# Kernel optimization log

Hardware: AMD Instinct MI355X
Metric: run time of the kernel (lower is better)

The kernel has to match this reference:

```python
import jax, jax.numpy as jnp
import numpy as np

N_VARS = 50000
N_EDGES = 400000
HIDDEN = 128


def setup_inputs() -> dict:
    key = jax.random.key(0)
    k1, k2, k3 = jax.random.split(key, 3)
    x = jax.random.normal(k1, (N_VARS, HIDDEN), dtype=jnp.float32)
    # torch Linear(2H, H, bias=False): weight shape [H, 2H]
    W = jax.random.normal(k2, (HIDDEN, 2 * HIDDEN), dtype=jnp.float32) * (1.0 / np.sqrt(2 * HIDDEN))
    edge_idx = jax.random.randint(k3, (2, N_EDGES), 0, N_VARS, dtype=jnp.int32)
    return {"x": x, "W": W, "edge_idx": edge_idx}


def reference(x, W, edge_idx):
    # Symmetrize edges: append reversed edges -> [2, 2E]
    src = jnp.concatenate([edge_idx[0], edge_idx[1]])  # [2E]
    dst = jnp.concatenate([edge_idx[1], edge_idx[0]])  # [2E]
    # Gather endpoint features and concat -> [2E, 2H]
    m = jnp.concatenate([x[src], x[dst]], axis=1)
    # Small dense linear (no bias): [2E, 2H] @ [2H, H] -> [2E, H]
    m = m @ W.T
    # scatter_sum over destination index, dim_size = num_vars
    r = jax.ops.segment_sum(m, dst, num_segments=x.shape[0])
    return r
```

## Files before the change

### kernel.cpp

```cpp
#include <hip/hip_runtime.h>

#define N_VARS   50000
#define N_EDGES  400000
#define HID      128
#define MTILES   (N_VARS / 16)
#define GEMM_BLOCKS ((MTILES + 1) / 2)
#define NBKT_A   196
#define CCAP     4608
#define NBKT_G   1563
#define CAP      64
#define CAPP     66
#define ABLOCKS  391

#define Y1_B0   0
#define Y1_SZ   (N_VARS * HID)
#define Y2_B0   (Y1_B0 + Y1_SZ)
#define Y2_SZ   (N_VARS * HID * 2)
#define WB_B0   (Y2_B0 + Y2_SZ)
#define WB_SZ   (64 * 64 * 8 * 2)
#define INT_B0  (WB_B0 + WB_SZ)

#define I_GCOUNT 0
#define I_COARSE (I_GCOUNT + NBKT_A)

typedef __attribute__((ext_vector_type(8))) short bf16x8;
typedef __attribute__((ext_vector_type(4))) float f32x4;
typedef __attribute__((ext_vector_type(2))) float f32x2;

__device__ __forceinline__ unsigned short f2bf(float f) {
    unsigned u = __builtin_bit_cast(unsigned, f);
    unsigned r = u + 0x7fffu + ((u >> 16) & 1u);
    return (unsigned short)(r >> 16);
}

__device__ __forceinline__ bf16x8 cvt8(float4 a0, float4 a1) {
    bf16x8 r;
    r[0] = (short)f2bf(a0.x); r[1] = (short)f2bf(a0.y);
    r[2] = (short)f2bf(a0.z); r[3] = (short)f2bf(a0.w);
    r[4] = (short)f2bf(a1.x); r[5] = (short)f2bf(a1.y);
    r[6] = (short)f2bf(a1.z); r[7] = (short)f2bf(a1.w);
    return r;
}

__global__ __launch_bounds__(256) void prep_kernel(const float* __restrict__ W,
                                                   short* __restrict__ wb,
                                                   int* __restrict__ gcount) {
    int gid = blockIdx.x * 256 + threadIdx.x;
    if (gid < NBKT_A) gcount[gid] = 0;
    if (gid < 4096) {
        int f = gid >> 6, lane = gid & 63;
        int nt = f >> 2, kc = f & 3;
        int ml = lane & 15, quad = lane >> 4;
        int n = nt * 16 + ml;
        const float* wp = (n < HID) ? (W + (size_t)n * 256)
                                    : (W + (size_t)(n - HID) * 256 + HID);
        wp += kc * 32 + quad * 8;
        const float4* w4 = (const float4*)wp;
        *(bf16x8*)(wb + (size_t)f * 512 + lane * 8) = cvt8(w4[0], w4[1]);
    }
}

__global__ __launch_bounds__(256) void gemm_binA_kernel(
    const float* __restrict__ x, const short* __restrict__ wb,
    const int* __restrict__ e,
    unsigned char* __restrict__ y1f8, unsigned short* __restrict__ y2b,
    int* __restrict__ gcount, int* __restrict__ coarse) {
    __shared__ int cnt[NBKT_A];
    __shared__ int base[NBKT_A];
    const int t = threadIdx.x;

    if (blockIdx.x < GEMM_BLOCKS) {
        const int lane = t & 63;
        const int wv   = t >> 6;
        const int ml   = lane & 15;
        const int quad = lane >> 4;

        bf16x8 bfrag[4][4];
#pragma unroll
        for (int i = 0; i < 4; ++i)
#pragma unroll
            for (int kc = 0; kc < 4; ++kc)
                bfrag[i][kc] = *(const bf16x8*)(wb + (size_t)((wv * 4 + i) * 4 + kc) * 512 + lane * 8);

#pragma unroll
        for (int mi = 0; mi < 2; ++mi) {
            const int mt = blockIdx.x * 2 + mi;
            if (mt >= MTILES) break;
            const int v = mt * 16 + ml;

            bf16x8 afrag[4];
#pragma unroll
            for (int kc = 0; kc < 4; ++kc) {
                const float4* ap = (const float4*)(x + (size_t)v * HID + kc * 32 + quad * 8);
                afrag[kc] = cvt8(ap[0], ap[1]);
            }

            f32x4 acc[4];
#pragma unroll
            for (int i = 0; i < 4; ++i) acc[i] = f32x4{0.f, 0.f, 0.f, 0.f};
#pragma unroll
            for (int kc = 0; kc < 4; ++kc)
#pragma unroll
                for (int i = 0; i < 4; ++i)
                    acc[i] = __builtin_amdgcn_mfma_f32_16x16x32_bf16(bfrag[i][kc], afrag[kc], acc[i], 0, 0, 0);

            if (wv < 2) {
#pragma unroll
                for (int i = 0; i < 4; ++i) {
                    int w = __builtin_amdgcn_cvt_pk_fp8_f32(acc[i][0], acc[i][1], 0, false);
                    w     = __builtin_amdgcn_cvt_pk_fp8_f32(acc[i][2], acc[i][3], w, true);
                    *(int*)(y1f8 + (size_t)v * HID + wv * 64 + i * 16 + quad * 4) = w;
                }
            } else {
#pragma unroll
                for (int i = 0; i < 4; ++i) {
                    uint2 p;
                    p.x = (unsigned)f2bf(acc[i][0]) | ((unsigned)f2bf(acc[i][1]) << 16);
                    p.y = (unsigned)f2bf(acc[i][2]) | ((unsigned)f2bf(acc[i][3]) << 16);
                    *(uint2*)(y2b + (size_t)v * HID + (wv - 2) * 64 + i * 16 + quad * 4) = p;
                }
            }
        }
    } else {
        const int bA = blockIdx.x - GEMM_BLOCKS;
        if (t < NBKT_A) cnt[t] = 0;
        __syncthreads();

        int e0[4], e1[4], nb = 0;
        const int b0 = (bA * 256 + t) * 4;
        if (bA < ABLOCKS - 1) {
            int4 A = *(const int4*)(e + b0);
            int4 B = *(const int4*)(e + N_EDGES + b0);
            e0[0] = A.x; e0[1] = A.y; e0[2] = A.z; e0[3] = A.w;
            e1[0] = B.x; e1[1] = B.y; e1[2] = B.z; e1[3] = B.w;
            nb = 4;
        } else {
            for (int j = 0; j < 4; ++j)
                if (b0 + j < N_EDGES) { e0[nb] = e[b0 + j]; e1[nb] = e[N_EDGES + b0 + j]; ++nb; }
        }

        int bkt[8], lpos[8], pk[8];
#pragma unroll 4
        for (int j = 0; j < nb; ++j) {
            int a = e0[j], b = e1[j];
            bkt[2 * j]      = b >> 8;
            pk[2 * j]       = (a << 8) | (b & 255);
            lpos[2 * j]     = atomicAdd(&cnt[b >> 8], 1);
            bkt[2 * j + 1]  = a >> 8;
            pk[2 * j + 1]   = (b << 8) | (a & 255);
            lpos[2 * j + 1] = atomicAdd(&cnt[a >> 8], 1);
        }
        __syncthreads();
        if (t < NBKT_A)
            base[t] = (cnt[t] > 0) ? atomicAdd(&gcount[t], cnt[t]) : 0;
        __syncthreads();

        for (int j = 0; j < 2 * nb; ++j) {
            int p = base[bkt[j]] + lpos[j];
            if (p < CCAP) coarse[bkt[j] * CCAP + p] = pk[j];
        }
    }
}

__global__ __launch_bounds__(256) void gather_kernel(
    const unsigned char* __restrict__ y1f8,
    const unsigned short* __restrict__ y2b,
    const int* __restrict__ gcount,
    const int* __restrict__ coarse,
    float* __restrict__ out) {
    __shared__ int fcnt[32];
    __shared__ unsigned short fine[32 * CAPP];
    const int t = threadIdx.x, b = blockIdx.x;
    const int parent = b >> 3, sub = b & 7;
    if (t < 32) fcnt[t] = 0;
    __syncthreads();

    int n = gcount[parent];
    if (n > CCAP) n = CCAP;
    const int* cb = coarse + (size_t)parent * CCAP;
    for (int i = t; i < n; i += 256) {
        int p = cb[i];
        if (((p >> 5) & 7) == sub) {
            int dl = p & 31;
            int pos = atomicAdd(&fcnt[dl], 1);
            if (pos < CAP) fine[dl * CAPP + pos] = (unsigned short)((unsigned)p >> 8);
        }
    }
    __syncthreads();

    const int g    = t >> 3;
    const int lane = t & 7;
    const int v    = b * 32 + g;
    if (v >= N_VARS) return;
    const int c = fcnt[g];
    const int nn = (c < CAP) ? c : CAP;
    const unsigned short* bucket = fine + g * CAPP;

    const uint4* base = (const uint4*)y1f8;
    float acc[16];
#pragma unroll
    for (int i = 0; i < 16; ++i) acc[i] = 0.f;

    auto accum = [&](uint4 a) {
        int u[4] = {(int)a.x, (int)a.y, (int)a.z, (int)a.w};
#pragma unroll
        for (int w = 0; w < 4; ++w) {
            f32x2 lo = __builtin_amdgcn_cvt_pk_f32_fp8(u[w], false);
            f32x2 hi = __builtin_amdgcn_cvt_pk_f32_fp8(u[w], true);
            acc[4 * w + 0] += lo[0];
            acc[4 * w + 1] += lo[1];
            acc[4 * w + 2] += hi[0];
            acc[4 * w + 3] += hi[1];
        }
    };

    int j = 0;
    for (; j + 4 <= nn; j += 4) {
        int s0 = bucket[j + 0], s1 = bucket[j + 1];
        int s2 = bucket[j + 2], s3 = bucket[j + 3];
        uint4 a0 = base[(size_t)s0 * 8 + lane];
        uint4 a1 = base[(size_t)s1 * 8 + lane];
        uint4 a2 = base[(size_t)s2 * 8 + lane];
        uint4 a3 = base[(size_t)s3 * 8 + lane];
        accum(a0); accum(a1); accum(a2); accum(a3);
    }
    for (; j < nn; ++j) accum(base[(size_t)bucket[j] * 8 + lane]);

    const uint4* y2p = (const uint4*)(y2b + (size_t)v * HID) + lane * 2;
    uint4 w0 = y2p[0], w1 = y2p[1];
    unsigned uu[8] = {w0.x, w0.y, w0.z, w0.w, w1.x, w1.y, w1.z, w1.w};
    const float dg = (float)c;
    float4* op = (float4*)(out + (size_t)v * HID + lane * 16);
#pragma unroll
    for (int q = 0; q < 4; ++q) {
        float b0 = __builtin_bit_cast(float, uu[2 * q] << 16);
        float b1 = __builtin_bit_cast(float, uu[2 * q] & 0xffff0000u);
        float b2 = __builtin_bit_cast(float, uu[2 * q + 1] << 16);
        float b3 = __builtin_bit_cast(float, uu[2 * q + 1] & 0xffff0000u);
        float4 o = {dg * b0 + acc[4 * q + 0], dg * b1 + acc[4 * q + 1],
                    dg * b2 + acc[4 * q + 2], dg * b3 + acc[4 * q + 3]};
        op[q] = o;
    }
}

extern "C" void kernel_launch(void* const* d_in, const int* in_sizes, int n_in,
                              void* d_out, int out_size, void* d_ws, size_t ws_size,
                              hipStream_t stream) {
    const float* x = (const float*)d_in[0];
    const float* W = (const float*)d_in[1];
    const int*   e = (const int*)d_in[2];
    float* out = (float*)d_out;

    unsigned char* wsb = (unsigned char*)d_ws;
    unsigned char*  y1f8   = wsb + Y1_B0;
    unsigned short* y2b    = (unsigned short*)(wsb + Y2_B0);
    short*          wb     = (short*)(wsb + WB_B0);
    int*            wsi    = (int*)(wsb + INT_B0);
    int*            gcount = wsi + I_GCOUNT;
    int*            coarse = wsi + I_COARSE;

    prep_kernel<<<17, 256, 0, stream>>>(W, wb, gcount);
    gemm_binA_kernel<<<GEMM_BLOCKS + ABLOCKS, 256, 0, stream>>>(
        x, wb, e, y1f8, y2b, gcount, coarse);
    gather_kernel<<<NBKT_G, 256, 0, stream>>>(y1f8, y2b, gcount, coarse, out);
}
```

Before: 125.0 us.

## Use hardware bf16 pack, prefetch both GEMM tiles, unroll gather loop by eight

```diff
diff --git a/kernel.cpp b/kernel.cpp
--- a/kernel.cpp
+++ b/kernel.cpp
@@ -27,19 +27,19 @@
 typedef __attribute__((ext_vector_type(4))) float f32x4;
 typedef __attribute__((ext_vector_type(2))) float f32x2;
 
-__device__ __forceinline__ unsigned short f2bf(float f) {
-    unsigned u = __builtin_bit_cast(unsigned, f);
-    unsigned r = u + 0x7fffu + ((u >> 16) & 1u);
-    return (unsigned short)(r >> 16);
+__device__ __forceinline__ unsigned pk_bf16(float lo, float hi) {
+    unsigned r;
+    asm("v_cvt_pk_bf16_f32 %0, %1, %2" : "=v"(r) : "v"(lo), "v"(hi));
+    return r;
 }
 
 __device__ __forceinline__ bf16x8 cvt8(float4 a0, float4 a1) {
-    bf16x8 r;
-    r[0] = (short)f2bf(a0.x); r[1] = (short)f2bf(a0.y);
-    r[2] = (short)f2bf(a0.z); r[3] = (short)f2bf(a0.w);
-    r[4] = (short)f2bf(a1.x); r[5] = (short)f2bf(a1.y);
-    r[6] = (short)f2bf(a1.z); r[7] = (short)f2bf(a1.w);
-    return r;
+    union { bf16x8 v; unsigned u[4]; } r;
+    r.u[0] = pk_bf16(a0.x, a0.y);
+    r.u[1] = pk_bf16(a0.z, a0.w);
+    r.u[2] = pk_bf16(a1.x, a1.y);
+    r.u[3] = pk_bf16(a1.z, a1.w);
+    return r.v;
 }
 
 __global__ __launch_bounds__(256) void prep_kernel(const float* __restrict__ W,
@@ -82,18 +82,33 @@
             for (int kc = 0; kc < 4; ++kc)
                 bfrag[i][kc] = *(const bf16x8*)(wb + (size_t)((wv * 4 + i) * 4 + kc) * 512 + lane * 8);
 
+        const int mt0 = blockIdx.x * 2;
+        const bool hasB = (mt0 + 1 < MTILES);
+        const int v0 = mt0 * 16 + ml;
+        const int v1 = hasB ? (mt0 + 1) * 16 + ml : v0;
+
+        float4 a[8], bq[8];
+#pragma unroll
+        for (int kc = 0; kc < 4; ++kc) {
+            const float4* ap = (const float4*)(x + (size_t)v0 * HID + kc * 32 + quad * 8);
+            a[2 * kc] = ap[0]; a[2 * kc + 1] = ap[1];
+        }
+#pragma unroll
+        for (int kc = 0; kc < 4; ++kc) {
+            const float4* bp = (const float4*)(x + (size_t)v1 * HID + kc * 32 + quad * 8);
+            bq[2 * kc] = bp[0]; bq[2 * kc + 1] = bp[1];
+        }
+        bf16x8 afA[4], afB[4];
+#pragma unroll
+        for (int kc = 0; kc < 4; ++kc) afA[kc] = cvt8(a[2 * kc], a[2 * kc + 1]);
+#pragma unroll
+        for (int kc = 0; kc < 4; ++kc) afB[kc] = cvt8(bq[2 * kc], bq[2 * kc + 1]);
+
 #pragma unroll
         for (int mi = 0; mi < 2; ++mi) {
-            const int mt = blockIdx.x * 2 + mi;
-            if (mt >= MTILES) break;
-            const int v = mt * 16 + ml;
-
-            bf16x8 afrag[4];
-#pragma unroll
-            for (int kc = 0; kc < 4; ++kc) {
-                const float4* ap = (const float4*)(x + (size_t)v * HID + kc * 32 + quad * 8);
-                afrag[kc] = cvt8(ap[0], ap[1]);
-            }
+            if (mi == 1 && !hasB) break;
+            const int v = mi ? v1 : v0;
+            const bf16x8* af = mi ? afB : afA;
 
             f32x4 acc[4];
 #pragma unroll
@@ -102,7 +117,7 @@
             for (int kc = 0; kc < 4; ++kc)
 #pragma unroll
                 for (int i = 0; i < 4; ++i)
-                    acc[i] = __builtin_amdgcn_mfma_f32_16x16x32_bf16(bfrag[i][kc], afrag[kc], acc[i], 0, 0, 0);
+                    acc[i] = __builtin_amdgcn_mfma_f32_16x16x32_bf16(bfrag[i][kc], af[kc], acc[i], 0, 0, 0);
 
             if (wv < 2) {
 #pragma unroll
@@ -115,8 +130,8 @@
 #pragma unroll
                 for (int i = 0; i < 4; ++i) {
                     uint2 p;
-                    p.x = (unsigned)f2bf(acc[i][0]) | ((unsigned)f2bf(acc[i][1]) << 16);
-                    p.y = (unsigned)f2bf(acc[i][2]) | ((unsigned)f2bf(acc[i][3]) << 16);
+                    p.x = pk_bf16(acc[i][0], acc[i][1]);
+                    p.y = pk_bf16(acc[i][2], acc[i][3]);
                     *(uint2*)(y2b + (size_t)v * HID + (wv - 2) * 64 + i * 16 + quad * 4) = p;
                 }
             }
@@ -215,6 +230,16 @@
     };
 
     int j = 0;
+    for (; j + 8 <= nn; j += 8) {
+        int s[8];
+#pragma unroll
+        for (int q = 0; q < 8; ++q) s[q] = bucket[j + q];
+        uint4 av[8];
+#pragma unroll
+        for (int q = 0; q < 8; ++q) av[q] = base[(size_t)s[q] * 8 + lane];
+#pragma unroll
+        for (int q = 0; q < 8; ++q) accum(av[q]);
+    }
     for (; j + 4 <= nn; j += 4) {
         int s0 = bucket[j + 0], s1 = bucket[j + 1];
         int s2 = bucket[j + 2], s3 = bucket[j + 3];
```

Result: slower. 142.4 us (+14.0%).
